# Kernel optimization log

Hardware: AMD Instinct MI355X
Metric: run time of the kernel (lower is better)

The kernel has to match this reference:

```python
import jax, jax.numpy as jnp
import numpy as np

B, H, S, D = 2, 16, 2048, 64
MASK_NEG = 1e9


def setup_inputs() -> dict:
    key = jax.random.key(0)
    kq, kk, kv, km = jax.random.split(key, 4)
    Q = jax.random.normal(kq, (B, H, S, D), dtype=jnp.float32)
    K = jax.random.normal(kk, (B, H, S, D), dtype=jnp.float32)
    V = jax.random.normal(kv, (B, H, S, D), dtype=jnp.float32)
    # float 0/1 mask, broadcast over heads; 1 = masked-out position
    attn_mask = jax.random.randint(km, (B, 1, S, S), 0, 2).astype(jnp.float32)
    return {"Q": Q, "K": K, "V": V, "attn_mask": attn_mask}


def reference(Q, K, V, attn_mask):
    # scores: [B, H, S, S]
    attn_score = jnp.einsum('bhqd,bhkd->bhqk', Q, K)
    scale = jnp.sqrt(jnp.asarray(K.shape[-1], dtype=jnp.float32))
    attn_scale = attn_score / scale - MASK_NEG * attn_mask
    attn_prob = jax.nn.softmax(attn_scale, axis=-1)
    attn_out = jnp.einsum('bhqk,bhkd->bhqd', attn_prob, V)
    return attn_out
```

## Files before the change

kernel.cpp:

```cpp
#include <hip/hip_runtime.h>


#define S_LEN 2048
#define D_DIM 64
#define BM    128
#define BN    64
#define WPR   32
#define NIT   32

typedef __attribute__((ext_vector_type(8))) short bf16x8;
typedef __attribute__((ext_vector_type(4))) float f32x4;
typedef unsigned long long ull;

__device__ __forceinline__ f32x4 mfma16(bf16x8 a, bf16x8 b, f32x4 c) {
  return __builtin_amdgcn_mfma_f32_16x16x32_bf16(a, b, c, 0, 0, 0);
}
__device__ __forceinline__ unsigned short f2bf(float f) {
  unsigned u = __builtin_bit_cast(unsigned, f);
  unsigned r = u + 0x7FFFu + ((u >> 16) & 1u);
  return (unsigned short)(r >> 16);
}
__device__ __forceinline__ float bf2f(unsigned short s) {
  unsigned u = ((unsigned)s) << 16;
  return __builtin_bit_cast(float, u);
}
__device__ __forceinline__ float fexp2(float x) {
#if __has_builtin(__builtin_amdgcn_exp2f)
  return __builtin_amdgcn_exp2f(x);
#else
  return exp2f(x);
#endif
}
__device__ __forceinline__ bool detect_bf16(const void* maskp) {
  const unsigned short* s = (const unsigned short*)maskp;
  unsigned short v = s[2 * (threadIdx.x & 63)];
  return __ballot(v == (unsigned short)0x3F80) != 0ull;
}
__device__ __forceinline__ int4 cvt_f8(const float* p) {
  float4 f0 = *(const float4*)p;
  float4 f1 = *(const float4*)(p + 4);
  int4 r;
  r.x = (unsigned)f2bf(f0.x) | ((unsigned)f2bf(f0.y) << 16);
  r.y = (unsigned)f2bf(f0.z) | ((unsigned)f2bf(f0.w) << 16);
  r.z = (unsigned)f2bf(f1.x) | ((unsigned)f2bf(f1.y) << 16);
  r.w = (unsigned)f2bf(f1.z) | ((unsigned)f2bf(f1.w) << 16);
  return r;
}
__device__ __forceinline__ void gload16(unsigned short* lds, const unsigned short* g) {
  __builtin_amdgcn_global_load_lds(
      (const __attribute__((address_space(1))) void*)g,
      (__attribute__((address_space(3))) void*)lds, 16, 0, 0);
}

#define C1 0.18033688011112042f
#define C2 1.4426950408889634e9f

__global__ __launch_bounds__(256) void prep_bits_k(
    const void* __restrict__ M, const void* __restrict__ Kin,
    ull* __restrict__ bits, unsigned short* __restrict__ Kc) {
  bool isb = detect_bf16(M);
  unsigned bx = blockIdx.x;
  if (bx < 32768u) {
    unsigned idx = bx * 256u + threadIdx.x;
    bool on = isb ? (bf2f(((const unsigned short*)M)[idx]) > 0.5f)
                  : (((const float*)M)[idx] > 0.5f);
    ull bm = __ballot(on);
    if ((threadIdx.x & 63u) == 0u) {
      unsigned c = idx & 2047u, r = (idx >> 11) & 2047u, bb = idx >> 22;
      bits[(((size_t)(bb * WPR + (c >> 6))) << 11) + r] = bm;
    }
  } else {
    size_t i0 = ((size_t)(bx - 32768u) * 256 + threadIdx.x) * 8;
    if (isb) {
      *(int4*)&Kc[i0] = *(const int4*)((const unsigned short*)Kin + i0);
    } else {
      *(int4*)&Kc[i0] = cvt_f8((const float*)Kin + i0);
    }
  }
}

__global__ __launch_bounds__(256) void transpose_v(
    const void* __restrict__ Vin, const void* __restrict__ maskp,
    unsigned short* __restrict__ Vo) {
  __shared__ __align__(16) unsigned short T[64 * 72];
  bool isb = detect_bf16(maskp);
  const int bh = blockIdx.y;
  const int k0 = blockIdx.x * 64;
  const int tid = threadIdx.x;
  {
    int k = tid >> 2, d0 = (tid & 3) * 16;
    unsigned short v[16];
    if (isb) {
      const unsigned short* src = (const unsigned short*)Vin +
          (size_t)bh * S_LEN * D_DIM + (size_t)(k0 + k) * D_DIM + d0;
      *(int4*)v = *(const int4*)src;
      *(int4*)(v + 8) = *(const int4*)(src + 8);
    } else {
      const float* src = (const float*)Vin +
          (size_t)bh * S_LEN * D_DIM + (size_t)(k0 + k) * D_DIM + d0;
      *(int4*)v = cvt_f8(src);
      *(int4*)(v + 8) = cvt_f8(src + 8);
    }
    *(int4*)&T[k * 72 + d0] = *(int4*)v;
    *(int4*)&T[k * 72 + d0 + 8] = *(int4*)(v + 8);
  }
  __syncthreads();
  {
    int d = tid >> 2, kg = (tid & 3) * 16;
    unsigned short v[16];
    #pragma unroll
    for (int j = 0; j < 16; ++j) v[j] = T[(kg + j) * 72 + d];
    unsigned short* dst = Vo + (size_t)bh * D_DIM * S_LEN + (size_t)d * S_LEN + k0 + kg;
    *(int4*)dst = *(int4*)v;
    *(int4*)(dst + 8) = *(int4*)(v + 8);
  }
}

__global__ __launch_bounds__(256, 2) void attn_fast(
    const void* __restrict__ Qp, const unsigned short* __restrict__ Kc,
    const unsigned short* __restrict__ Vt, const ull* __restrict__ bits,
    const void* __restrict__ maskp, void* __restrict__ Op) {
  __shared__ __align__(16) unsigned short Klds[2][64 * 64];
  __shared__ __align__(16) unsigned short Vlds[2][64 * 64];
  __shared__ __align__(16) unsigned short Plds[128 * 72];

  const bool isb = detect_bf16(maskp);
  const int tid  = threadIdx.x;
  const int wave = tid >> 6;
  const int lane = tid & 63;
  const int l15  = lane & 15;
  const int quad = lane >> 4;
  const int rsw  = l15 & 7;
  const int q0   = blockIdx.x * BM;
  const int bh   = blockIdx.y;
  const int b    = bh >> 4;
  const size_t base = (size_t)bh * S_LEN * D_DIM;

  const unsigned short* Kg0 = Kc + base;
  const unsigned short* Vg0 = Vt + (size_t)bh * D_DIM * S_LEN;

  {
    #pragma unroll
    for (int p = 0; p < 2; ++p) {
      int s = p * 256 + tid;
      int r = s >> 3;
      int cg = (s & 7) ^ (r & 7);
      gload16(&Klds[0][s * 8], Kg0 + r * D_DIM + cg * 8);
      gload16(&Vlds[0][s * 8], Vg0 + r * S_LEN + cg * 8);
    }
  }

  bf16x8 qf[2][2];
  #pragma unroll
  for (int mi = 0; mi < 2; ++mi)
    #pragma unroll
    for (int kt = 0; kt < 2; ++kt) {
      size_t off = base + (size_t)(q0 + wave * 32 + mi * 16 + l15) * D_DIM + kt * 32 + quad * 8;
      unsigned short v[8];
      if (isb) {
        *(int4*)v = *(const int4*)((const unsigned short*)Qp + off);
        #pragma unroll
        for (int j = 0; j < 8; ++j) v[j] = f2bf(bf2f(v[j]) * C1);
      } else {
        const float* f = (const float*)Qp + off;
        float4 f0 = *(const float4*)f;
        float4 f1 = *(const float4*)(f + 4);
        v[0] = f2bf(f0.x * C1); v[1] = f2bf(f0.y * C1);
        v[2] = f2bf(f0.z * C1); v[3] = f2bf(f0.w * C1);
        v[4] = f2bf(f1.x * C1); v[5] = f2bf(f1.y * C1);
        v[6] = f2bf(f1.z * C1); v[7] = f2bf(f1.w * C1);
      }
      qf[mi][kt] = *(const bf16x8*)v;
    }

  f32x4 acc_o[2][4];
  f32x4 acc_l[2];
  const f32x4 zero4 = {0.f, 0.f, 0.f, 0.f};
  #pragma unroll
  for (int mi = 0; mi < 2; ++mi) {
    acc_l[mi] = zero4;
    #pragma unroll
    for (int nt = 0; nt < 4; ++nt) acc_o[mi][nt] = zero4;
  }
  bf16x8 onesB;
  {
    short ov = (l15 == 0) ? (short)0x3F80 : (short)0;
    #pragma unroll
    for (int i = 0; i < 8; ++i) onesB[i] = ov;
  }

  int cur = 0;
  for (int it = 0; it < NIT; ++it) {
    __syncthreads();

    if (it + 1 < NIT) {
      const unsigned short* Kg = Kg0 + (size_t)(it + 1) * BN * D_DIM;
      const unsigned short* Vg = Vg0 + (it + 1) * BN;
      unsigned short* Kl = Klds[cur ^ 1];
      unsigned short* Vl = Vlds[cur ^ 1];
      #pragma unroll
      for (int p = 0; p < 2; ++p) {
        int s = p * 256 + tid;
        int r = s >> 3;
        int cg = (s & 7) ^ (r & 7);
        gload16(Kl + s * 8, Kg + r * D_DIM + cg * 8);
        gload16(Vl + s * 8, Vg + r * S_LEN + cg * 8);
      }
    }

    unsigned mlo[2][4], mhi[2][4];
    {
      const ull* bw = bits + (((size_t)(b * WPR + it)) << 11) + q0 + wave * 32;
      #pragma unroll
      for (int mi = 0; mi < 2; ++mi) {
        ulonglong2 a = *(const ulonglong2*)(bw + mi * 16 + quad * 4);
        ulonglong2 c = *(const ulonglong2*)(bw + mi * 16 + quad * 4 + 2);
        ull w0 = a.x >> l15, w1 = a.y >> l15, w2 = c.x >> l15, w3 = c.y >> l15;
        mlo[mi][0] = (unsigned)w0; mhi[mi][0] = (unsigned)(w0 >> 32);
        mlo[mi][1] = (unsigned)w1; mhi[mi][1] = (unsigned)(w1 >> 32);
        mlo[mi][2] = (unsigned)w2; mhi[mi][2] = (unsigned)(w2 >> 32);
        mlo[mi][3] = (unsigned)w3; mhi[mi][3] = (unsigned)(w3 >> 32);
      }
    }

    const unsigned short* Kl = Klds[cur];
    const unsigned short* Vl = Vlds[cur];

    #pragma unroll
    for (int nt = 0; nt < 4; ++nt) {
      const int krow = (nt * 16 + l15) * 64;
      bf16x8 kf0 = *(const bf16x8*)&Kl[krow + (quad ^ rsw) * 8];
      bf16x8 kf1 = *(const bf16x8*)&Kl[krow + ((4 + quad) ^ rsw) * 8];
      f32x4 s0 = zero4, s1 = zero4;
      s0 = mfma16(qf[0][0], kf0, s0);
      s0 = mfma16(qf[0][1], kf1, s0);
      s1 = mfma16(qf[1][0], kf0, s1);
      s1 = mfma16(qf[1][1], kf1, s1);
      #pragma unroll
      for (int mi = 0; mi < 2; ++mi) {
        f32x4 sv = mi ? s1 : s0;
        #pragma unroll
        for (int reg = 0; reg < 4; ++reg) {
          float p = fexp2(sv[reg]);
          unsigned bit = (nt < 2) ? ((mlo[mi][reg] >> (nt * 16)) & 1u)
                                  : ((mhi[mi][reg] >> ((nt - 2) * 16)) & 1u);
          if (bit) p = 0.0f;
          Plds[(wave * 32 + mi * 16 + quad * 4 + reg) * 72 + nt * 16 + l15] =
              (short)f2bf(p);
        }
      }
    }

    #pragma unroll
    for (int kt = 0; kt < 2; ++kt) {
      bf16x8 pf0 = *(const bf16x8*)&Plds[(wave * 32 + l15) * 72 + kt * 32 + quad * 8];
      bf16x8 pf1 = *(const bf16x8*)&Plds[(wave * 32 + 16 + l15) * 72 + kt * 32 + quad * 8];
      #pragma unroll
      for (int nt = 0; nt < 4; ++nt) {
        int drow = (nt * 16 + l15) * 64;
        bf16x8 vf = *(const bf16x8*)&Vl[drow + ((kt * 4 + quad) ^ rsw) * 8];
        acc_o[0][nt] = mfma16(pf0, vf, acc_o[0][nt]);
        acc_o[1][nt] = mfma16(pf1, vf, acc_o[1][nt]);
      }
      acc_l[0] = mfma16(pf0, onesB, acc_l[0]);
      acc_l[1] = mfma16(pf1, onesB, acc_l[1]);
    }
    cur ^= 1;
  }

  #pragma unroll
  for (int mi = 0; mi < 2; ++mi) {
    #pragma unroll
    for (int reg = 0; reg < 4; ++reg) {
      float lv = __shfl(acc_l[mi][reg], lane & 48, 64);
      float inv = 1.0f / lv;
      #pragma unroll
      for (int nt = 0; nt < 4; ++nt) {
        float o = acc_o[mi][nt][reg] * inv;
        size_t idx = base +
            (size_t)(q0 + wave * 32 + mi * 16 + quad * 4 + reg) * D_DIM + nt * 16 + l15;
        if (isb) ((unsigned short*)Op)[idx] = f2bf(o);
        else     ((float*)Op)[idx] = o;
      }
    }
  }
}

__global__ __launch_bounds__(256, 2) void attn_fallback(
    const void* __restrict__ Qp, const void* __restrict__ Kp,
    const void* __restrict__ Vp, const void* __restrict__ maskp,
    void* __restrict__ Op) {
  __shared__ __align__(16) short QKlds[BM * 72];
  __shared__ __align__(16) short Vtlds[D_DIM * 72];
  __shared__ __align__(16) short Plds2[BM * 72];

  const bool isb = detect_bf16(maskp);
  const int tid  = threadIdx.x;
  const int wave = tid >> 6;
  const int lane = tid & 63;
  const int l15  = lane & 15;
  const int quad = lane >> 4;
  const int q0   = blockIdx.x * BM;
  const int bh   = blockIdx.y;
  const int b    = bh >> 4;
  const size_t base = (size_t)bh * S_LEN * D_DIM;

  const short* Qs = (const short*)Qp; const float* Qf = (const float*)Qp;
  const short* Ks = (const short*)Kp; const float* Kf = (const float*)Kp;
  const short* Vs = (const short*)Vp; const float* Vf = (const float*)Vp;

  if (isb) {
    const short* Qg = Qs + base + (size_t)q0 * D_DIM;
    #pragma unroll
    for (int p = 0; p < 4; ++p) {
      int e = p * 2048 + tid * 8;
      *(int4*)&QKlds[(e >> 6) * 72 + (e & 63)] = *(const int4*)(Qg + e);
    }
  } else {
    const float* Qg = Qf + base + (size_t)q0 * D_DIM;
    #pragma unroll
    for (int p = 0; p < 4; ++p) {
      int e = p * 2048 + tid * 8;
      *(int4*)&QKlds[(e >> 6) * 72 + (e & 63)] = cvt_f8(Qg + e);
    }
  }
  __syncthreads();
  bf16x8 qf[2][2];
  #pragma unroll
  for (int mi = 0; mi < 2; ++mi)
    #pragma unroll
    for (int kt = 0; kt < 2; ++kt)
      qf[mi][kt] = *(const bf16x8*)&QKlds[(wave * 32 + mi * 16 + l15) * 72 + kt * 32 + quad * 8];
  __syncthreads();

  f32x4 acc_o[2][4];
  f32x4 acc_l[2];
  const f32x4 zero4 = {0.f, 0.f, 0.f, 0.f};
  #pragma unroll
  for (int mi = 0; mi < 2; ++mi) {
    acc_l[mi] = zero4;
    #pragma unroll
    for (int nt = 0; nt < 4; ++nt) acc_o[mi][nt] = zero4;
  }
  bf16x8 onesB;
  {
    short ov = (l15 == 0) ? (short)0x3F80 : (short)0;
    #pragma unroll
    for (int i = 0; i < 8; ++i) onesB[i] = ov;
  }

  for (int it = 0; it < NIT; ++it) {
    const int k0 = it * BN;
    if (isb) {
      const short* Kg = Ks + base + (size_t)k0 * D_DIM;
      #pragma unroll
      for (int p = 0; p < 2; ++p) {
        int e = p * 2048 + tid * 8;
        *(int4*)&QKlds[(e >> 6) * 72 + (e & 63)] = *(const int4*)(Kg + e);
      }
    } else {
      const float* Kg = Kf + base + (size_t)k0 * D_DIM;
      #pragma unroll
      for (int p = 0; p < 2; ++p) {
        int e = p * 2048 + tid * 8;
        *(int4*)&QKlds[(e >> 6) * 72 + (e & 63)] = cvt_f8(Kg + e);
      }
    }
    {
      const int r0 = (tid >> 3) * 2;
      const int d0 = (tid & 7) * 8;
      unsigned short as_[8], bs_[8];
      if (isb) {
        const short* Vg = Vs + base + (size_t)k0 * D_DIM;
        *(int4*)as_ = *(const int4*)(Vg + r0 * D_DIM + d0);
        *(int4*)bs_ = *(const int4*)(Vg + (r0 + 1) * D_DIM + d0);
      } else {
        const float* Vg = Vf + base + (size_t)k0 * D_DIM;
        *(int4*)as_ = cvt_f8(Vg + r0 * D_DIM + d0);
        *(int4*)bs_ = cvt_f8(Vg + (r0 + 1) * D_DIM + d0);
      }
      #pragma unroll
      for (int j = 0; j < 8; ++j) {
        int d = d0 + j;
        int blk = (r0 >> 3) ^ (d >> 3);
        unsigned pk = (unsigned)as_[j] | ((unsigned)bs_[j] << 16);
        *(unsigned*)&Vtlds[d * 72 + blk * 8 + (r0 & 7)] = pk;
      }
    }
    __syncthreads();

    f32x4 sc[2][4];
    #pragma unroll
    for (int mi = 0; mi < 2; ++mi)
      #pragma unroll
      for (int nt = 0; nt < 4; ++nt) sc[mi][nt] = zero4;
    #pragma unroll
    for (int nt = 0; nt < 4; ++nt) {
      bf16x8 kf0 = *(const bf16x8*)&QKlds[(nt * 16 + l15) * 72 + quad * 8];
      bf16x8 kf1 = *(const bf16x8*)&QKlds[(nt * 16 + l15) * 72 + 32 + quad * 8];
      #pragma unroll
      for (int mi = 0; mi < 2; ++mi) {
        sc[mi][nt] = mfma16(qf[mi][0], kf0, sc[mi][nt]);
        sc[mi][nt] = mfma16(qf[mi][1], kf1, sc[mi][nt]);
      }
    }

    #pragma unroll
    for (int mi = 0; mi < 2; ++mi) {
      #pragma unroll
      for (int nt = 0; nt < 4; ++nt) {
        #pragma unroll
        for (int reg = 0; reg < 4; ++reg) {
          int rg = q0 + wave * 32 + mi * 16 + quad * 4 + reg;
          size_t mix = (size_t)b * S_LEN * S_LEN + (size_t)rg * S_LEN + k0 + nt * 16 + l15;
          float mv = isb ? bf2f(((const unsigned short*)maskp)[mix])
                         : ((const float*)maskp)[mix];
          float y = sc[mi][nt][reg] * C1 - mv * C2;
          Plds2[(wave * 32 + mi * 16 + quad * 4 + reg) * 72 + nt * 16 + l15] =
              (short)f2bf(fexp2(y));
        }
      }
    }
    __syncthreads();

    #pragma unroll
    for (int kt = 0; kt < 2; ++kt) {
      bf16x8 pf[2];
      #pragma unroll
      for (int mi = 0; mi < 2; ++mi)
        pf[mi] = *(const bf16x8*)&Plds2[(wave * 32 + mi * 16 + l15) * 72 + kt * 32 + quad * 8];
      #pragma unroll
      for (int nt = 0; nt < 4; ++nt) {
        int d = nt * 16 + l15;
        int kb = (kt * 4 + quad) ^ (d >> 3);
        bf16x8 vf = *(const bf16x8*)&Vtlds[d * 72 + kb * 8];
        #pragma unroll
        for (int mi = 0; mi < 2; ++mi)
          acc_o[mi][nt] = mfma16(pf[mi], vf, acc_o[mi][nt]);
      }
      #pragma unroll
      for (int mi = 0; mi < 2; ++mi)
        acc_l[mi] = mfma16(pf[mi], onesB, acc_l[mi]);
    }
    __syncthreads();
  }

  #pragma unroll
  for (int mi = 0; mi < 2; ++mi) {
    #pragma unroll
    for (int reg = 0; reg < 4; ++reg) {
      float lv = __shfl(acc_l[mi][reg], lane & 48, 64);
      float inv = 1.0f / lv;
      #pragma unroll
      for (int nt = 0; nt < 4; ++nt) {
        float o = acc_o[mi][nt][reg] * inv;
        size_t idx = base + (size_t)(q0 + wave * 32 + mi * 16 + quad * 4 + reg) * D_DIM + nt * 16 + l15;
        if (isb) ((unsigned short*)Op)[idx] = f2bf(o);
        else     ((float*)Op)[idx] = o;
      }
    }
  }
}

extern "C" void kernel_launch(void* const* d_in, const int* in_sizes, int n_in,
                              void* d_out, int out_size, void* d_ws, size_t ws_size,
                              hipStream_t stream) {
  const void* Q = d_in[0];
  const void* K = d_in[1];
  const void* V = d_in[2];
  const void* M = d_in[3];

  dim3 block(256);
  const size_t bits_bytes = (size_t)2 * S_LEN * S_LEN / 8;
  const size_t tens_bytes = (size_t)2 * 16 * S_LEN * D_DIM * 2;

  if (ws_size >= bits_bytes + 2 * tens_bytes) {
    char* ws = (char*)d_ws;
    ull* bits = (ull*)ws;
    unsigned short* Kc = (unsigned short*)(ws + bits_bytes);
    unsigned short* Vc = (unsigned short*)(ws + bits_bytes + tens_bytes);
    prep_bits_k<<<dim3(32768 + 2048), block, 0, stream>>>(M, K, bits, Kc);
    transpose_v<<<dim3(S_LEN / 64, 32), block, 0, stream>>>(V, M, Vc);
    attn_fast<<<dim3(S_LEN / BM, 32), block, 0, stream>>>(Q, Kc, Vc, bits, M, d_out);
  } else {
    attn_fallback<<<dim3(S_LEN / BM, 32), block, 0, stream>>>(Q, K, V, M, d_out);
  }
}
```

Baseline: 198.7 us.

## Pre-swizzle K/V into MFMA fragment layout and split key range across wave pairs

The prep kernels merge into one launch that writes K and V already arranged in per-lane MFMA fragment order. The attention kernel then loads K/V fragments straight from global memory into registers, dropping the LDS double-buffering and its block-wide barriers. Each block now covers 64 query rows, with two waves splitting the 32 key tiles and combining partial O and row-sum through LDS at the end. This removes one launch and the per-iteration syncs and raises occupancy, but every wave now makes redundant global loads of K/V and the waves lose LDS sharing.

```diff
diff --git a/kernel.cpp b/kernel.cpp
--- a/kernel.cpp
+++ b/kernel.cpp
@@ -3,8 +3,6 @@
 
 #define S_LEN 2048
 #define D_DIM 64
-#define BM    128
-#define BN    64
 #define WPR   32
 #define NIT   32
 
@@ -46,83 +44,81 @@
   r.w = (unsigned)f2bf(f1.z) | ((unsigned)f2bf(f1.w) << 16);
   return r;
 }
-__device__ __forceinline__ void gload16(unsigned short* lds, const unsigned short* g) {
-  __builtin_amdgcn_global_load_lds(
-      (const __attribute__((address_space(1))) void*)g,
-      (__attribute__((address_space(3))) void*)lds, 16, 0, 0);
-}
 
 #define C1 0.18033688011112042f
 #define C2 1.4426950408889634e9f
 
-__global__ __launch_bounds__(256) void prep_bits_k(
+__global__ __launch_bounds__(256) void prep_all(
     const void* __restrict__ M, const void* __restrict__ Kin,
-    ull* __restrict__ bits, unsigned short* __restrict__ Kc) {
-  bool isb = detect_bf16(M);
-  unsigned bx = blockIdx.x;
+    const void* __restrict__ Vin, ull* __restrict__ bits,
+    unsigned short* __restrict__ Kf, unsigned short* __restrict__ Vf) {
+  __shared__ __align__(16) unsigned short T[64 * 72];
+  const bool isb = detect_bf16(M);
+  const unsigned bx = blockIdx.x;
+  const int tid = threadIdx.x;
+
   if (bx < 32768u) {
-    unsigned idx = bx * 256u + threadIdx.x;
+    unsigned idx = bx * 256u + tid;
     bool on = isb ? (bf2f(((const unsigned short*)M)[idx]) > 0.5f)
                   : (((const float*)M)[idx] > 0.5f);
     ull bm = __ballot(on);
-    if ((threadIdx.x & 63u) == 0u) {
+    if ((tid & 63) == 0) {
       unsigned c = idx & 2047u, r = (idx >> 11) & 2047u, bb = idx >> 22;
       bits[(((size_t)(bb * WPR + (c >> 6))) << 11) + r] = bm;
     }
+  } else if (bx < 32768u + 2048u) {
+    unsigned g = (bx - 32768u) * 256u + tid;
+    unsigned lane = g & 63u;
+    unsigned f = (g >> 6) & 7u;
+    unsigned ti = (g >> 9) & 31u;
+    unsigned bh = g >> 14;
+    unsigned nt = f >> 1, kt = f & 1;
+    unsigned quad = lane >> 4, l15 = lane & 15;
+    size_t src = (size_t)bh * (S_LEN * D_DIM) +
+                 (size_t)(ti * 64 + nt * 16 + l15) * D_DIM + kt * 32 + quad * 8;
+    int4 out;
+    if (isb) out = *(const int4*)((const unsigned short*)Kin + src);
+    else     out = cvt_f8((const float*)Kin + src);
+    *(int4*)&Kf[(size_t)g * 8] = out;
   } else {
-    size_t i0 = ((size_t)(bx - 32768u) * 256 + threadIdx.x) * 8;
-    if (isb) {
-      *(int4*)&Kc[i0] = *(const int4*)((const unsigned short*)Kin + i0);
-    } else {
-      *(int4*)&Kc[i0] = cvt_f8((const float*)Kin + i0);
-    }
-  }
-}
-
-__global__ __launch_bounds__(256) void transpose_v(
-    const void* __restrict__ Vin, const void* __restrict__ maskp,
-    unsigned short* __restrict__ Vo) {
-  __shared__ __align__(16) unsigned short T[64 * 72];
-  bool isb = detect_bf16(maskp);
-  const int bh = blockIdx.y;
-  const int k0 = blockIdx.x * 64;
-  const int tid = threadIdx.x;
-  {
-    int k = tid >> 2, d0 = (tid & 3) * 16;
-    unsigned short v[16];
-    if (isb) {
-      const unsigned short* src = (const unsigned short*)Vin +
-          (size_t)bh * S_LEN * D_DIM + (size_t)(k0 + k) * D_DIM + d0;
-      *(int4*)v = *(const int4*)src;
-      *(int4*)(v + 8) = *(const int4*)(src + 8);
-    } else {
-      const float* src = (const float*)Vin +
-          (size_t)bh * S_LEN * D_DIM + (size_t)(k0 + k) * D_DIM + d0;
-      *(int4*)v = cvt_f8(src);
-      *(int4*)(v + 8) = cvt_f8(src + 8);
-    }
-    *(int4*)&T[k * 72 + d0] = *(int4*)v;
-    *(int4*)&T[k * 72 + d0 + 8] = *(int4*)(v + 8);
-  }
-  __syncthreads();
-  {
-    int d = tid >> 2, kg = (tid & 3) * 16;
-    unsigned short v[16];
-    #pragma unroll
-    for (int j = 0; j < 16; ++j) v[j] = T[(kg + j) * 72 + d];
-    unsigned short* dst = Vo + (size_t)bh * D_DIM * S_LEN + (size_t)d * S_LEN + k0 + kg;
-    *(int4*)dst = *(int4*)v;
-    *(int4*)(dst + 8) = *(int4*)(v + 8);
-  }
-}
-
-__global__ __launch_bounds__(256, 2) void attn_fast(
-    const void* __restrict__ Qp, const unsigned short* __restrict__ Kc,
-    const unsigned short* __restrict__ Vt, const ull* __restrict__ bits,
+    unsigned idx = bx - (32768u + 2048u);
+    unsigned bh = idx >> 5, ti = idx & 31u;
+    {
+      int k = tid >> 2, d0 = (tid & 3) * 16;
+      size_t src = (size_t)bh * (S_LEN * D_DIM) + (size_t)(ti * 64 + k) * D_DIM + d0;
+      int4 a, c;
+      if (isb) {
+        const unsigned short* s = (const unsigned short*)Vin + src;
+        a = *(const int4*)s; c = *(const int4*)(s + 8);
+      } else {
+        const float* s = (const float*)Vin + src;
+        a = cvt_f8(s); c = cvt_f8(s + 8);
+      }
+      *(int4*)&T[k * 72 + d0] = a;
+      *(int4*)&T[k * 72 + d0 + 8] = c;
+    }
+    __syncthreads();
+    #pragma unroll
+    for (int h = 0; h < 2; ++h) {
+      int c = tid + h * 256;
+      int lane = c & 63, f = c >> 6;
+      int kt = f >> 2, nt = f & 3;
+      int quad = lane >> 4, l15 = lane & 15;
+      unsigned short v[8];
+      #pragma unroll
+      for (int j = 0; j < 8; ++j)
+        v[j] = T[(kt * 32 + quad * 8 + j) * 72 + nt * 16 + l15];
+      *(int4*)&Vf[(((size_t)(bh * 32 + ti)) * 8 + f) * 512 + lane * 8] = *(int4*)v;
+    }
+  }
+}
+
+__global__ __launch_bounds__(256, 4) void attn_fast(
+    const void* __restrict__ Qp, const unsigned short* __restrict__ Kf,
+    const unsigned short* __restrict__ Vf, const ull* __restrict__ bits,
     const void* __restrict__ maskp, void* __restrict__ Op) {
-  __shared__ __align__(16) unsigned short Klds[2][64 * 64];
-  __shared__ __align__(16) unsigned short Vlds[2][64 * 64];
-  __shared__ __align__(16) unsigned short Plds[128 * 72];
+  __shared__ __align__(16) unsigned short Plds[4 * 32 * 72];
+  __shared__ __align__(16) f32x4 Lcomb[2][8];
 
   const bool isb = detect_bf16(maskp);
   const int tid  = threadIdx.x;
@@ -130,32 +126,20 @@
   const int lane = tid & 63;
   const int l15  = lane & 15;
   const int quad = lane >> 4;
-  const int rsw  = l15 & 7;
-  const int q0   = blockIdx.x * BM;
+  const int pair = wave >> 1;
+  const int half = wave & 1;
+  const int q0   = blockIdx.x * 64;
   const int bh   = blockIdx.y;
   const int b    = bh >> 4;
   const size_t base = (size_t)bh * S_LEN * D_DIM;
-
-  const unsigned short* Kg0 = Kc + base;
-  const unsigned short* Vg0 = Vt + (size_t)bh * D_DIM * S_LEN;
-
-  {
-    #pragma unroll
-    for (int p = 0; p < 2; ++p) {
-      int s = p * 256 + tid;
-      int r = s >> 3;
-      int cg = (s & 7) ^ (r & 7);
-      gload16(&Klds[0][s * 8], Kg0 + r * D_DIM + cg * 8);
-      gload16(&Vlds[0][s * 8], Vg0 + r * S_LEN + cg * 8);
-    }
-  }
+  const int rows0 = q0 + pair * 32;
 
   bf16x8 qf[2][2];
   #pragma unroll
   for (int mi = 0; mi < 2; ++mi)
     #pragma unroll
     for (int kt = 0; kt < 2; ++kt) {
-      size_t off = base + (size_t)(q0 + wave * 32 + mi * 16 + l15) * D_DIM + kt * 32 + quad * 8;
+      size_t off = base + (size_t)(rows0 + mi * 16 + l15) * D_DIM + kt * 32 + quad * 8;
       unsigned short v[8];
       if (isb) {
         *(int4*)v = *(const int4*)((const unsigned short*)Qp + off);
@@ -189,28 +173,27 @@
     for (int i = 0; i < 8; ++i) onesB[i] = ov;
   }
 
-  int cur = 0;
-  for (int it = 0; it < NIT; ++it) {
-    __syncthreads();
-
-    if (it + 1 < NIT) {
-      const unsigned short* Kg = Kg0 + (size_t)(it + 1) * BN * D_DIM;
-      const unsigned short* Vg = Vg0 + (it + 1) * BN;
-      unsigned short* Kl = Klds[cur ^ 1];
-      unsigned short* Vl = Vlds[cur ^ 1];
-      #pragma unroll
-      for (int p = 0; p < 2; ++p) {
-        int s = p * 256 + tid;
-        int r = s >> 3;
-        int cg = (s & 7) ^ (r & 7);
-        gload16(Kl + s * 8, Kg + r * D_DIM + cg * 8);
-        gload16(Vl + s * 8, Vg + r * S_LEN + cg * 8);
-      }
-    }
+  unsigned short* Pw = Plds + wave * (32 * 72);
+  const int it0 = half * 16;
+
+  for (int it = it0; it < it0 + 16; ++it) {
+    const unsigned short* Kb = Kf + (((size_t)(bh * 32 + it)) * 8) * 512 + lane * 8;
+    const unsigned short* Vb = Vf + (((size_t)(bh * 32 + it)) * 8) * 512 + lane * 8;
+    bf16x8 kfr[4][2], vfr[2][4];
+    #pragma unroll
+    for (int nt = 0; nt < 4; ++nt)
+      #pragma unroll
+      for (int kt = 0; kt < 2; ++kt)
+        kfr[nt][kt] = *(const bf16x8*)(Kb + (nt * 2 + kt) * 512);
+    #pragma unroll
+    for (int kt = 0; kt < 2; ++kt)
+      #pragma unroll
+      for (int nt = 0; nt < 4; ++nt)
+        vfr[kt][nt] = *(const bf16x8*)(Vb + (kt * 4 + nt) * 512);
 
     unsigned mlo[2][4], mhi[2][4];
     {
-      const ull* bw = bits + (((size_t)(b * WPR + it)) << 11) + q0 + wave * 32;
+      const ull* bw = bits + (((size_t)(b * WPR + it)) << 11) + rows0;
       #pragma unroll
       for (int mi = 0; mi < 2; ++mi) {
         ulonglong2 a = *(const ulonglong2*)(bw + mi * 16 + quad * 4);
@@ -223,19 +206,13 @@
       }
     }
 
-    const unsigned short* Kl = Klds[cur];
-    const unsigned short* Vl = Vlds[cur];
-
     #pragma unroll
     for (int nt = 0; nt < 4; ++nt) {
-      const int krow = (nt * 16 + l15) * 64;
-      bf16x8 kf0 = *(const bf16x8*)&Kl[krow + (quad ^ rsw) * 8];
-      bf16x8 kf1 = *(const bf16x8*)&Kl[krow + ((4 + quad) ^ rsw) * 8];
       f32x4 s0 = zero4, s1 = zero4;
-      s0 = mfma16(qf[0][0], kf0, s0);
-      s0 = mfma16(qf[0][1], kf1, s0);
-      s1 = mfma16(qf[1][0], kf0, s1);
-      s1 = mfma16(qf[1][1], kf1, s1);
+      s0 = mfma16(qf[0][0], kfr[nt][0], s0);
+      s0 = mfma16(qf[0][1], kfr[nt][1], s0);
+      s1 = mfma16(qf[1][0], kfr[nt][0], s1);
+      s1 = mfma16(qf[1][1], kfr[nt][1], s1);
       #pragma unroll
       for (int mi = 0; mi < 2; ++mi) {
         f32x4 sv = mi ? s1 : s0;
@@ -245,42 +222,54 @@
           unsigned bit = (nt < 2) ? ((mlo[mi][reg] >> (nt * 16)) & 1u)
                                   : ((mhi[mi][reg] >> ((nt - 2) * 16)) & 1u);
           if (bit) p = 0.0f;
-          Plds[(wave * 32 + mi * 16 + quad * 4 + reg) * 72 + nt * 16 + l15] =
-              (short)f2bf(p);
+          Pw[(mi * 16 + quad * 4 + reg) * 72 + nt * 16 + l15] = (short)f2bf(p);
         }
       }
     }
 
     #pragma unroll
     for (int kt = 0; kt < 2; ++kt) {
-      bf16x8 pf0 = *(const bf16x8*)&Plds[(wave * 32 + l15) * 72 + kt * 32 + quad * 8];
-      bf16x8 pf1 = *(const bf16x8*)&Plds[(wave * 32 + 16 + l15) * 72 + kt * 32 + quad * 8];
+      bf16x8 pf0 = *(const bf16x8*)&Pw[(l15) * 72 + kt * 32 + quad * 8];
+      bf16x8 pf1 = *(const bf16x8*)&Pw[(16 + l15) * 72 + kt * 32 + quad * 8];
       #pragma unroll
       for (int nt = 0; nt < 4; ++nt) {
-        int drow = (nt * 16 + l15) * 64;
-        bf16x8 vf = *(const bf16x8*)&Vl[drow + ((kt * 4 + quad) ^ rsw) * 8];
-        acc_o[0][nt] = mfma16(pf0, vf, acc_o[0][nt]);
-        acc_o[1][nt] = mfma16(pf1, vf, acc_o[1][nt]);
+        acc_o[0][nt] = mfma16(pf0, vfr[kt][nt], acc_o[0][nt]);
+        acc_o[1][nt] = mfma16(pf1, vfr[kt][nt], acc_o[1][nt]);
       }
       acc_l[0] = mfma16(pf0, onesB, acc_l[0]);
       acc_l[1] = mfma16(pf1, onesB, acc_l[1]);
     }
-    cur ^= 1;
-  }
-
-  #pragma unroll
-  for (int mi = 0; mi < 2; ++mi) {
-    #pragma unroll
-    for (int reg = 0; reg < 4; ++reg) {
-      float lv = __shfl(acc_l[mi][reg], lane & 48, 64);
-      float inv = 1.0f / lv;
-      #pragma unroll
-      for (int nt = 0; nt < 4; ++nt) {
-        float o = acc_o[mi][nt][reg] * inv;
-        size_t idx = base +
-            (size_t)(q0 + wave * 32 + mi * 16 + quad * 4 + reg) * D_DIM + nt * 16 + l15;
-        if (isb) ((unsigned short*)Op)[idx] = f2bf(o);
-        else     ((float*)Op)[idx] = o;
+  }
+
+  __syncthreads();
+  f32x4* Pc = (f32x4*)Plds;
+  if (half == 1) {
+    #pragma unroll
+    for (int mi = 0; mi < 2; ++mi) {
+      #pragma unroll
+      for (int nt = 0; nt < 4; ++nt)
+        Pc[(size_t)(pair * 8 + mi * 4 + nt) * 64 + lane] = acc_o[mi][nt];
+      if (l15 == 0) Lcomb[pair][mi * 4 + quad] = acc_l[mi];
+    }
+  }
+  __syncthreads();
+  if (half == 0) {
+    #pragma unroll
+    for (int mi = 0; mi < 2; ++mi) {
+      #pragma unroll
+      for (int nt = 0; nt < 4; ++nt)
+        acc_o[mi][nt] += Pc[(size_t)(pair * 8 + mi * 4 + nt) * 64 + lane];
+      #pragma unroll
+      for (int reg = 0; reg < 4; ++reg) {
+        float lv = __shfl(acc_l[mi][reg], lane & 48, 64) + Lcomb[pair][mi * 4 + quad][reg];
+        float inv = 1.0f / lv;
+        #pragma unroll
+        for (int nt = 0; nt < 4; ++nt) {
+          float o = acc_o[mi][nt][reg] * inv;
+          size_t idx = base + (size_t)(rows0 + mi * 16 + quad * 4 + reg) * D_DIM + nt * 16 + l15;
+          if (isb) ((unsigned short*)Op)[idx] = f2bf(o);
+          else     ((float*)Op)[idx] = o;
+        }
       }
     }
   }
@@ -290,9 +279,9 @@
     const void* __restrict__ Qp, const void* __restrict__ Kp,
     const void* __restrict__ Vp, const void* __restrict__ maskp,
     void* __restrict__ Op) {
-  __shared__ __align__(16) short QKlds[BM * 72];
-  __shared__ __align__(16) short Vtlds[D_DIM * 72];
-  __shared__ __align__(16) short Plds2[BM * 72];
+  __shared__ __align__(16) short QKlds[128 * 72];
+  __shared__ __align__(16) short Vtlds[64 * 72];
+  __shared__ __align__(16) short Plds2[128 * 72];
 
   const bool isb = detect_bf16(maskp);
   const int tid  = threadIdx.x;
@@ -300,14 +289,14 @@
   const int lane = tid & 63;
   const int l15  = lane & 15;
   const int quad = lane >> 4;
-  const int q0   = blockIdx.x * BM;
+  const int q0   = blockIdx.x * 128;
   const int bh   = blockIdx.y;
   const int b    = bh >> 4;
   const size_t base = (size_t)bh * S_LEN * D_DIM;
 
   const short* Qs = (const short*)Qp; const float* Qf = (const float*)Qp;
-  const short* Ks = (const short*)Kp; const float* Kf = (const float*)Kp;
-  const short* Vs = (const short*)Vp; const float* Vf = (const float*)Vp;
+  const short* Ks = (const short*)Kp; const float* Kf2 = (const float*)Kp;
+  const short* Vs = (const short*)Vp; const float* Vf2 = (const float*)Vp;
 
   if (isb) {
     const short* Qg = Qs + base + (size_t)q0 * D_DIM;
@@ -350,7 +339,7 @@
   }
 
   for (int it = 0; it < NIT; ++it) {
-    const int k0 = it * BN;
+    const int k0 = it * 64;
     if (isb) {
       const short* Kg = Ks + base + (size_t)k0 * D_DIM;
       #pragma unroll
@@ -359,7 +348,7 @@
         *(int4*)&QKlds[(e >> 6) * 72 + (e & 63)] = *(const int4*)(Kg + e);
       }
     } else {
-      const float* Kg = Kf + base + (size_t)k0 * D_DIM;
+      const float* Kg = Kf2 + base + (size_t)k0 * D_DIM;
       #pragma unroll
       for (int p = 0; p < 2; ++p) {
         int e = p * 2048 + tid * 8;
@@ -375,7 +364,7 @@
         *(int4*)as_ = *(const int4*)(Vg + r0 * D_DIM + d0);
         *(int4*)bs_ = *(const int4*)(Vg + (r0 + 1) * D_DIM + d0);
       } else {
-        const float* Vg = Vf + base + (size_t)k0 * D_DIM;
+        const float* Vg = Vf2 + base + (size_t)k0 * D_DIM;
         *(int4*)as_ = cvt_f8(Vg + r0 * D_DIM + d0);
         *(int4*)bs_ = cvt_f8(Vg + (r0 + 1) * D_DIM + d0);
       }
@@ -477,12 +466,11 @@
   if (ws_size >= bits_bytes + 2 * tens_bytes) {
     char* ws = (char*)d_ws;
     ull* bits = (ull*)ws;
-    unsigned short* Kc = (unsigned short*)(ws + bits_bytes);
-    unsigned short* Vc = (unsigned short*)(ws + bits_bytes + tens_bytes);
-    prep_bits_k<<<dim3(32768 + 2048), block, 0, stream>>>(M, K, bits, Kc);
-    transpose_v<<<dim3(S_LEN / 64, 32), block, 0, stream>>>(V, M, Vc);
-    attn_fast<<<dim3(S_LEN / BM, 32), block, 0, stream>>>(Q, Kc, Vc, bits, M, d_out);
+    unsigned short* Kf = (unsigned short*)(ws + bits_bytes);
+    unsigned short* Vf = (unsigned short*)(ws + bits_bytes + tens_bytes);
+    prep_all<<<dim3(32768 + 2048 + 1024), block, 0, stream>>>(M, K, V, bits, Kf, Vf);
+    attn_fast<<<dim3(S_LEN / 64, 32), block, 0, stream>>>(Q, Kf, Vf, bits, M, d_out);
   } else {
-    attn_fallback<<<dim3(S_LEN / BM, 32), block, 0, stream>>>(Q, K, V, M, d_out);
-  }
-}
+    attn_fallback<<<dim3(S_LEN / 128, 32), block, 0, stream>>>(Q, K, V, M, d_out);
+  }
+}
```

Result: faster. 190.5 us (-4.1%).
